# Kernel tuning notes

Measured on AMD Instinct MI355X. Metric: run time of the kernel, lower is better.

The kernel has to match this reference:

```python
import jax, jax.numpy as jnp
import numpy as np

MODES = 2
LC = 4
N = 6000
KNN = 10
NODES = 64
CH = MODES ** 2
M = N * 2 * (KNN + 1)  # total candidate couplings


def setup_inputs() -> dict:
    key = jax.random.key(0)
    ks = jax.random.split(key, 6)
    return {
        "CK_inputs": jax.random.normal(ks[0], (N, 2 * (KNN + 1), 3), dtype=jnp.float32),
        "W_in": jax.random.normal(ks[1], (3, NODES), dtype=jnp.float32) * 0.1,
        "b_in": jnp.zeros((NODES,), dtype=jnp.float32),
        "W_hid": jax.random.normal(ks[2], (LC - 1, NODES, NODES), dtype=jnp.float32) * 0.1,
        "b_hid": jnp.zeros((LC - 1, NODES), dtype=jnp.float32),
        "W_out": jax.random.normal(ks[3], (NODES, CH), dtype=jnp.float32) * 0.1,
        "b_out": jnp.zeros((CH,), dtype=jnp.float32),
        "coo": jax.random.randint(ks[4], (2, M), 0, N, dtype=jnp.int32),
    }


def _mlp(x, W_in, b_in, W_hid, b_hid, W_out, b_out):
    # MLP: 3 -> 64, (LC-1) hidden 64->64 layers, 64 -> CH; ReLU activations.
    h = jax.nn.relu(x @ W_in + b_in)
    for i in range(W_hid.shape[0]):  # small fixed layer count
        h = jax.nn.relu(h @ W_hid[i] + b_hid[i])
    return h @ W_out + b_out  # [M, CH]


def reference(CK_inputs, W_in, b_in, W_hid, b_hid, W_out, b_out, coo):
    C_stripped = _mlp(CK_inputs.reshape(-1, 3), W_in, b_in, W_hid, b_hid, W_out, b_out)  # [M, CH]
    D = MODES * N
    # Original: for channel ch = mi*MODES+mj, scatter C_stripped[:, ch] at indices coo*MODES+mj
    # (mj added to BOTH row and col, replicating the source exactly). Indices are
    # independent of mi, so sum over mi first, then one scatter-add per mj.
    vals = C_stripped.reshape(-1, MODES, MODES).sum(axis=1)  # [M, MODES]; axis1=mi, axis2=mj
    dense = jnp.zeros((D, D), dtype=CK_inputs.dtype)
    for mj in range(MODES):
        idx = coo * MODES + mj  # [2, M]
        dense = dense.at[idx[0], idx[1]].add(vals[:, mj])
    return dense
```

## Files before the change

kernel.cpp:

```cpp
#include <hip/hip_runtime.h>
#include <stdint.h>

#define NN    6000
#define KNNC  10
#define MM    (NN * 2 * (KNNC + 1))
#define DD    (2 * NN)
#define LCH   3
#define BLK   256

__global__ __launch_bounds__(BLK) void fused_mlp_zero(
    const float* __restrict__ CK,
    const float* __restrict__ Win,
    const float* __restrict__ bin,
    const float* __restrict__ Whid,
    const float* __restrict__ bhid,
    const float* __restrict__ Wout,
    const float* __restrict__ bout,
    float* __restrict__ vals,
    float* __restrict__ out)
{
    __shared__ float sWT[LCH * 4096];
    __shared__ float sWin[3 * 64];
    __shared__ float sBin[64];
    __shared__ float sBhid[LCH * 64];
    __shared__ float sWoutC[64 * 2];
    __shared__ float sBoutC[2];

    const int tid = threadIdx.x;

    {
        float4 z = make_float4(0.f, 0.f, 0.f, 0.f);
        float4* outv = (float4*)out;
        const long long NV = (long long)DD * DD / 4;
        long long i = (long long)blockIdx.x * BLK + tid;
        const long long stride = (long long)gridDim.x * BLK;
        for (; i < NV; i += stride) outv[i] = z;
    }

    if (tid < 192) {
        int l = tid >> 6, k = tid & 63;
        const float* src = Whid + (l * 64 + k) * 64;
        float* dst = sWT + l * 4096 + k;
        for (int j = 0; j < 64; j++) dst[j * 64] = src[j];
    }
    if (tid < 192) sWin[tid] = Win[tid];
    if (tid < 64)  sBin[tid] = bin[tid];
    if (tid < 192) sBhid[tid] = bhid[tid];
    if (tid < 64) {
        sWoutC[tid * 2 + 0] = Wout[tid * 4 + 0] + Wout[tid * 4 + 2];
        sWoutC[tid * 2 + 1] = Wout[tid * 4 + 1] + Wout[tid * 4 + 3];
    }
    if (tid < 2) sBoutC[tid] = bout[tid] + bout[tid + 2];
    __syncthreads();

    const int m = blockIdx.x * BLK + tid;
    if (m >= MM) return;

    const float x0 = CK[m * 3 + 0];
    const float x1 = CK[m * 3 + 1];
    const float x2 = CK[m * 3 + 2];

    float h[64];
#pragma unroll
    for (int j = 0; j < 64; j++) {
        float a = sBin[j] + x0 * sWin[j] + x1 * sWin[64 + j] + x2 * sWin[128 + j];
        h[j] = fmaxf(a, 0.0f);
    }

    for (int l = 0; l < LCH; l++) {
        const float* WT = sWT + (l << 12);
        const float* bh = sBhid + (l << 6);
        float g[64];
#pragma unroll
        for (int j = 0; j < 64; j++) {
            float acc = bh[j];
            const float4* w4 = (const float4*)(WT + (j << 6));
#pragma unroll
            for (int k4 = 0; k4 < 16; k4++) {
                float4 w = w4[k4];
                acc += h[k4 * 4 + 0] * w.x;
                acc += h[k4 * 4 + 1] * w.y;
                acc += h[k4 * 4 + 2] * w.z;
                acc += h[k4 * 4 + 3] * w.w;
            }
            g[j] = fmaxf(acc, 0.0f);
        }
#pragma unroll
        for (int j = 0; j < 64; j++) h[j] = g[j];
    }

    float v0 = sBoutC[0], v1 = sBoutC[1];
#pragma unroll
    for (int k = 0; k < 64; k++) {
        float2 wc = *(const float2*)(sWoutC + k * 2);
        v0 += h[k] * wc.x;
        v1 += h[k] * wc.y;
    }
    vals[m * 2 + 0] = v0;
    vals[m * 2 + 1] = v1;
}

__global__ __launch_bounds__(BLK) void scatter_add(
    const float* __restrict__ vals,
    const int* __restrict__ coo,
    float* __restrict__ out)
{
    const int t = blockIdx.x * BLK + threadIdx.x;
    if (t >= MM) return;
    const int r2 = coo[t] * 2;
    const int c2 = coo[MM + t] * 2;
    const float v0 = vals[t * 2 + 0];
    const float v1 = vals[t * 2 + 1];
    const long long f0 = (long long)r2 * DD + c2;
    atomicAdd(out + f0, v0);
    atomicAdd(out + f0 + DD + 1, v1);
}

extern "C" void kernel_launch(void* const* d_in, const int* in_sizes, int n_in,
                              void* d_out, int out_size, void* d_ws, size_t ws_size,
                              hipStream_t stream) {
    const float* CK   = (const float*)d_in[0];
    const float* Win  = (const float*)d_in[1];
    const float* bin  = (const float*)d_in[2];
    const float* Whid = (const float*)d_in[3];
    const float* bhid = (const float*)d_in[4];
    const float* Wout = (const float*)d_in[5];
    const float* bout = (const float*)d_in[6];
    const int* coo    = (const int*)d_in[7];
    float* out        = (float*)d_out;
    float* vals       = (float*)d_ws;

    const int blocks = (MM + BLK - 1) / BLK;

    fused_mlp_zero<<<blocks, BLK, 0, stream>>>(CK, Win, bin, Whid, bhid, Wout, bout, vals, out);
    scatter_add<<<blocks, BLK, 0, stream>>>(vals, coo, out);
}
```

Before: 755.7 us.

## Split zero-fill into dedicated blocks and read MLP weights directly from global

Result: faster. 711.4 us (-5.9%).

```diff
diff --git a/kernel.cpp b/kernel.cpp
--- a/kernel.cpp
+++ b/kernel.cpp
@@ -7,6 +7,9 @@
 #define DD    (2 * NN)
 #define LCH   3
 #define BLK   256
+
+#define MLP_BLOCKS  ((MM + BLK - 1) / BLK)
+#define FILL_BLOCKS 2048
 
 __global__ __launch_bounds__(BLK) void fused_mlp_zero(
     const float* __restrict__ CK,
@@ -19,39 +22,18 @@
     float* __restrict__ vals,
     float* __restrict__ out)
 {
-    __shared__ float sWT[LCH * 4096];
-    __shared__ float sWin[3 * 64];
-    __shared__ float sBin[64];
-    __shared__ float sBhid[LCH * 64];
-    __shared__ float sWoutC[64 * 2];
-    __shared__ float sBoutC[2];
-
     const int tid = threadIdx.x;
 
-    {
+    if (blockIdx.x >= MLP_BLOCKS) {
+        const int fb = blockIdx.x - MLP_BLOCKS;
         float4 z = make_float4(0.f, 0.f, 0.f, 0.f);
         float4* outv = (float4*)out;
         const long long NV = (long long)DD * DD / 4;
-        long long i = (long long)blockIdx.x * BLK + tid;
-        const long long stride = (long long)gridDim.x * BLK;
+        long long i = (long long)fb * BLK + tid;
+        const long long stride = (long long)FILL_BLOCKS * BLK;
         for (; i < NV; i += stride) outv[i] = z;
+        return;
     }
-
-    if (tid < 192) {
-        int l = tid >> 6, k = tid & 63;
-        const float* src = Whid + (l * 64 + k) * 64;
-        float* dst = sWT + l * 4096 + k;
-        for (int j = 0; j < 64; j++) dst[j * 64] = src[j];
-    }
-    if (tid < 192) sWin[tid] = Win[tid];
-    if (tid < 64)  sBin[tid] = bin[tid];
-    if (tid < 192) sBhid[tid] = bhid[tid];
-    if (tid < 64) {
-        sWoutC[tid * 2 + 0] = Wout[tid * 4 + 0] + Wout[tid * 4 + 2];
-        sWoutC[tid * 2 + 1] = Wout[tid * 4 + 1] + Wout[tid * 4 + 3];
-    }
-    if (tid < 2) sBoutC[tid] = bout[tid] + bout[tid + 2];
-    __syncthreads();
 
     const int m = blockIdx.x * BLK + tid;
     if (m >= MM) return;
@@ -63,38 +45,35 @@
     float h[64];
 #pragma unroll
     for (int j = 0; j < 64; j++) {
-        float a = sBin[j] + x0 * sWin[j] + x1 * sWin[64 + j] + x2 * sWin[128 + j];
+        float a = bin[j];
+        a = fmaf(x0, Win[j],       a);
+        a = fmaf(x1, Win[64 + j],  a);
+        a = fmaf(x2, Win[128 + j], a);
         h[j] = fmaxf(a, 0.0f);
     }
 
     for (int l = 0; l < LCH; l++) {
-        const float* WT = sWT + (l << 12);
-        const float* bh = sBhid + (l << 6);
+        const float* __restrict__ W  = Whid + (l << 12);
+        const float* __restrict__ bh = bhid + (l << 6);
         float g[64];
 #pragma unroll
-        for (int j = 0; j < 64; j++) {
-            float acc = bh[j];
-            const float4* w4 = (const float4*)(WT + (j << 6));
+        for (int j = 0; j < 64; j++) g[j] = bh[j];
+        for (int k = 0; k < 64; k++) {
+            const float hk = h[k];
+            const float* __restrict__ Wk = W + (k << 6);
 #pragma unroll
-            for (int k4 = 0; k4 < 16; k4++) {
-                float4 w = w4[k4];
-                acc += h[k4 * 4 + 0] * w.x;
-                acc += h[k4 * 4 + 1] * w.y;
-                acc += h[k4 * 4 + 2] * w.z;
-                acc += h[k4 * 4 + 3] * w.w;
-            }
-            g[j] = fmaxf(acc, 0.0f);
+            for (int j = 0; j < 64; j++) g[j] = fmaf(Wk[j], hk, g[j]);
         }
 #pragma unroll
-        for (int j = 0; j < 64; j++) h[j] = g[j];
+        for (int j = 0; j < 64; j++) h[j] = fmaxf(g[j], 0.0f);
     }
 
-    float v0 = sBoutC[0], v1 = sBoutC[1];
+    float v0 = bout[0] + bout[2];
+    float v1 = bout[1] + bout[3];
 #pragma unroll
     for (int k = 0; k < 64; k++) {
-        float2 wc = *(const float2*)(sWoutC + k * 2);
-        v0 += h[k] * wc.x;
-        v1 += h[k] * wc.y;
+        v0 = fmaf(h[k], Wout[k * 4 + 0] + Wout[k * 4 + 2], v0);
+        v1 = fmaf(h[k], Wout[k * 4 + 1] + Wout[k * 4 + 3], v1);
     }
     vals[m * 2 + 0] = v0;
     vals[m * 2 + 1] = v1;
@@ -130,8 +109,7 @@
     float* out        = (float*)d_out;
     float* vals       = (float*)d_ws;
 
-    const int blocks = (MM + BLK - 1) / BLK;
-
-    fused_mlp_zero<<<blocks, BLK, 0, stream>>>(CK, Win, bin, Whid, bhid, Wout, bout, vals, out);
-    scatter_add<<<blocks, BLK, 0, stream>>>(vals, coo, out);
+    fused_mlp_zero<<<MLP_BLOCKS + FILL_BLOCKS, BLK, 0, stream>>>(
+        CK, Win, bin, Whid, bhid, Wout, bout, vals, out);
+    scatter_add<<<MLP_BLOCKS, BLK, 0, stream>>>(vals, coo, out);
 }
```
